# Kernel optimization log

Measured on AMD Instinct MI355X. Metric: run time of the kernel, lower is better.

## Reference

```python
import jax, jax.numpy as jnp
import numpy as np

B, NA, NMAX, NC = 32, 8400, 32, 80
TOPK, ALPHA, BETA, EPS, BG_IDX = 13, 1.0, 6.0, 1e-9, 80
IMG = 640.0


def _ciou(box1, box2, eps=1e-7):
    # box1: (b, nmax, 1, 4) xyxy, box2: (b, 1, na, 4) xyxy -> CIoU (b, nmax, na)
    b1_x1, b1_y1, b1_x2, b1_y2 = (box1[..., 0], box1[..., 1], box1[..., 2], box1[..., 3])
    b2_x1, b2_y1, b2_x2, b2_y2 = (box2[..., 0], box2[..., 1], box2[..., 2], box2[..., 3])
    inter = (jnp.minimum(b1_x2, b2_x2) - jnp.maximum(b1_x1, b2_x1)).clip(0) * \
            (jnp.minimum(b1_y2, b2_y2) - jnp.maximum(b1_y1, b2_y1)).clip(0)
    w1, h1 = b1_x2 - b1_x1, b1_y2 - b1_y1 + eps
    w2, h2 = b2_x2 - b2_x1, b2_y2 - b2_y1 + eps
    union = w1 * h1 + w2 * h2 - inter + eps
    iou = inter / union
    cw = jnp.maximum(b1_x2, b2_x2) - jnp.minimum(b1_x1, b2_x1)
    ch = jnp.maximum(b1_y2, b2_y2) - jnp.minimum(b1_y1, b2_y1)
    c2 = cw * cw + ch * ch + eps
    rho2 = ((b2_x1 + b2_x2 - b1_x1 - b1_x2) ** 2 + (b2_y1 + b2_y2 - b1_y1 - b1_y2) ** 2) / 4.0
    v = (4.0 / np.pi ** 2) * (jnp.arctan(w2 / h2) - jnp.arctan(w1 / h1)) ** 2
    alpha = jax.lax.stop_gradient(v / (v - iou + (1.0 + eps)))
    return iou - (rho2 / c2 + v * alpha)


def _rand_boxes(key, shape):
    # well-formed xyxy boxes inside a 640x640 image
    k1, k2 = jax.random.split(key)
    xy = jax.random.uniform(k1, shape[:-1] + (2,), jnp.float32) * (IMG - 64.0)
    wh = jax.random.uniform(k2, shape[:-1] + (2,), jnp.float32) * 56.0 + 8.0
    return jnp.concatenate([xy, xy + wh], axis=-1)


def setup_inputs() -> dict:
    key = jax.random.key(0)
    ks = jax.random.split(key, 6)
    pd_scores = jax.random.uniform(ks[0], (B, NA, NC), jnp.float32)
    pd_bboxes = _rand_boxes(ks[1], (B, NA, 4))
    anc_points = jax.random.uniform(ks[2], (NA, 2), jnp.float32) * IMG
    gt_labels = jax.random.randint(ks[3], (B, NMAX, 1), 0, NC, dtype=jnp.int32)
    gt_bboxes = _rand_boxes(ks[4], (B, NMAX, 4))
    mask_gt = jnp.ones((B, NMAX, 1), jnp.float32)
    return {"pd_scores": pd_scores, "pd_bboxes": pd_bboxes, "anc_points": anc_points,
            "gt_labels": gt_labels, "gt_bboxes": gt_bboxes, "mask_gt": mask_gt}


def reference(pd_scores, pd_bboxes, anc_points, gt_labels, gt_bboxes, mask_gt):
    b, na, nc = pd_scores.shape
    nmax = gt_bboxes.shape[1]
    # pairwise CIoU between every GT and every predicted box: (b, nmax, na)
    overlaps = _ciou(gt_bboxes[:, :, None, :], pd_bboxes[:, None, :, :])
    # gather predicted class score at each GT's label: (b, nmax, na)
    p = jnp.transpose(pd_scores, (0, 2, 1))                     # (b, nc, na)
    scores = jnp.take_along_axis(p, gt_labels.astype(jnp.int32), axis=1)
    align_metric = (scores ** ALPHA) * (overlaps ** BETA)
    # top-k anchors per GT along the anchor axis, scatter to a boolean mask
    _, topk_idx = jax.lax.top_k(align_metric, TOPK)             # (b, nmax, topk)
    bi = jnp.arange(b)[:, None, None]
    gi = jnp.arange(nmax)[None, :, None]
    mask_pos = jnp.zeros((b, nmax, na), bool).at[bi, gi, topk_idx].set(True)
    target_gt_idx = jnp.argmax(mask_pos, axis=1)                # (b, na)
    fg_mask = mask_pos.sum(axis=1) > 0                          # (b, na)
    # gather assigned GT label / box per anchor
    target_labels = jnp.take_along_axis(gt_labels[..., 0].astype(jnp.int32), target_gt_idx, axis=1)
    target_bboxes = jnp.take_along_axis(gt_bboxes, target_gt_idx[..., None], axis=1)  # (b, na, 4)
    target_scores = jax.nn.one_hot(target_labels, nc, dtype=jnp.float32) * fg_mask[..., None]
    target_labels = jnp.where(fg_mask, target_labels, BG_IDX)
    # normalize target scores by mean positive overlap per anchor, clamped to [0, 1]
    mpf = mask_pos.astype(overlaps.dtype)
    pos_overlaps = jnp.clip((overlaps * mpf).sum(axis=1) / (mpf.sum(axis=1) + EPS), 0.0, 1.0)
    target_scores = target_scores * pos_overlaps[..., None]
    return target_labels, target_bboxes, target_scores, fg_mask, target_gt_idx
```

## Files before the change

kernel.cpp:

```cpp
#include <hip/hip_runtime.h>
#include <math.h>

#define BATCH 32
#define NA 8400
#define NMAX 32
#define NC 80
#define TOPK 13
#define THREADS 256
#define NF4ROW (NA / 4)
#define NPT4 9
#define TILE 128
#define NTILES 66
#define SSTRIDE 81

#define OFF_BOX 268800
#define OFF_SCR 1344000
#define OFF_FG  22848000
#define OFF_TGT 23116800
#define SCR_ELEMS (OFF_FG - OFF_SCR)
#define SCR_F4    (SCR_ELEMS / 4)
#define ZPB_M     2546

typedef float f32x4 __attribute__((ext_vector_type(4)));

__device__ __forceinline__ float ciou_f(float gx1, float gy1, float gx2, float gy2,
                                        float px1, float py1, float px2, float py2) {
    const float eps = 1e-7f;
    float iw = fmaxf(fminf(gx2, px2) - fmaxf(gx1, px1), 0.0f);
    float ih = fmaxf(fminf(gy2, py2) - fmaxf(gy1, py1), 0.0f);
    float inter = iw * ih;
    float w1 = gx2 - gx1, h1 = gy2 - gy1 + eps;
    float w2 = px2 - px1, h2 = py2 - py1 + eps;
    float uni = w1 * h1 + w2 * h2 - inter + eps;
    float iou = inter / uni;
    float cw = fmaxf(gx2, px2) - fminf(gx1, px1);
    float ch = fmaxf(gy2, py2) - fminf(gy1, py1);
    float c2 = cw * cw + ch * ch + eps;
    float dx = px1 + px2 - gx1 - gx2;
    float dy = py1 + py2 - gy1 - gy2;
    float rho2 = (dx * dx + dy * dy) / 4.0f;
    float dd = atanf(w2 / h2) - atanf(w1 / h1);
    float v = (float)(4.0 / (M_PI * M_PI)) * dd * dd;
    float alpha = v / (v - iou + (1.0f + eps));
    return iou - (rho2 / c2 + v * alpha);
}

__global__ __launch_bounds__(THREADS, 3) void metric_kernel(
    const float* __restrict__ pd_scores, const float* __restrict__ pd_bboxes,
    const int* __restrict__ gt_labels, const float* __restrict__ gt_bboxes,
    float* __restrict__ met, unsigned int* __restrict__ mask,
    float* __restrict__ zbase) {
    const int b = blockIdx.y;
    const int abase = blockIdx.x * TILE;
    const int tid = threadIdx.x;
    const int na_tile = min(TILE, NA - abase);
    const float eps = 1e-7f;

    if (tid < na_tile) mask[(size_t)b * NA + abase + tid] = 0u;

    __shared__ float ssc[TILE][SSTRIDE];
    __shared__ float4 spbox[TILE];
    __shared__ float sgx1[NMAX], sgy1[NMAX], sgx2[NMAX], sgy2[NMAX];
    __shared__ float sa1[NMAX], sat1[NMAX];
    __shared__ int   slbl[NMAX];

    if (tid < NMAX) {
        float4 g = ((const float4*)gt_bboxes)[b * NMAX + tid];
        float w1 = g.z - g.x, h1 = g.w - g.y + eps;
        sgx1[tid] = g.x; sgy1[tid] = g.y; sgx2[tid] = g.z; sgy2[tid] = g.w;
        sa1[tid]  = w1 * h1;
        sat1[tid] = atanf(w1 / h1);
        slbl[tid] = gt_labels[b * NMAX + tid];
    } else if (tid >= 128) {
        int al = tid - 128;
        if (al < na_tile)
            spbox[al] = ((const float4*)pd_bboxes)[(size_t)b * NA + abase + al];
    }

    const float4* srec4 = (const float4*)(pd_scores + ((size_t)b * NA + abase) * NC);
    const int nf4 = na_tile * 20;
    float4 r[10];
#pragma unroll
    for (int i = 0; i < 10; i++) {
        int f = tid + i * THREADS;
        if (f < nf4) r[i] = srec4[f];
    }
#pragma unroll
    for (int i = 0; i < 10; i++) {
        int f = tid + i * THREADS;
        if (f < nf4) {
            int a = f / 20, c = f % 20;
            float* d = &ssc[a][c * 4];
            d[0] = r[i].x; d[1] = r[i].y; d[2] = r[i].z; d[3] = r[i].w;
        }
    }
    __syncthreads();

    if (zbase) {
        const int bid = b * NTILES + blockIdx.x;
        const size_t zoff = (size_t)bid * ZPB_M;
        f32x4* zp = (f32x4*)zbase + zoff;
        const f32x4 z = { 0.f, 0.f, 0.f, 0.f };
#pragma unroll
        for (int i = 0; i < 10; i++) {
            int j = tid + i * THREADS;
            if (j < ZPB_M && zoff + j < SCR_F4)
                __builtin_nontemporal_store(z, zp + j);
        }
    }

    const int al = tid & (TILE - 1);
    const int gbase = (tid >> 7) * 16;
    if (al >= na_tile) return;

    float4 p = spbox[al];
    float w2 = p.z - p.x, h2 = p.w - p.y + eps;
    float a2  = w2 * h2;
    float at2 = atanf(w2 / h2);
    const size_t abs_a = (size_t)abase + al;

#pragma unroll
    for (int k = 0; k < 16; k++) {
        int gi = gbase + k;
        float gx1 = sgx1[gi], gy1 = sgy1[gi], gx2 = sgx2[gi], gy2 = sgy2[gi];
        float iw = fmaxf(fminf(gx2, p.z) - fmaxf(gx1, p.x), 0.0f);
        float ih = fmaxf(fminf(gy2, p.w) - fmaxf(gy1, p.y), 0.0f);
        float inter = iw * ih;
        float uni = sa1[gi] + a2 - inter + eps;
        float iou = inter / uni;
        float cw = fmaxf(gx2, p.z) - fminf(gx1, p.x);
        float ch = fmaxf(gy2, p.w) - fminf(gy1, p.y);
        float c2 = cw * cw + ch * ch + eps;
        float dx = p.x + p.z - gx1 - gx2;
        float dy = p.y + p.w - gy1 - gy2;
        float rho2 = (dx * dx + dy * dy) / 4.0f;
        float dd = at2 - sat1[gi];
        float v = (float)(4.0 / (M_PI * M_PI)) * dd * dd;
        float alpha = v / (v - iou + (1.0f + eps));
        float ov = iou - (rho2 / c2 + v * alpha);
        float sc = ssc[al][slbl[gi]];
        float ov2 = ov * ov;
        met[((size_t)b * NMAX + gi) * NA + abs_a] = sc * (ov2 * ov2 * ov2);
    }
}

__global__ __launch_bounds__(THREADS) void topk_kernel(
    const float* __restrict__ met, unsigned int* __restrict__ mask) {
    const int tid  = threadIdx.x;
    const int lane = tid & 63;
    const int w    = tid >> 6;
    const int bid  = blockIdx.x;
    const int b  = bid >> 5;
    const int gi = bid & 31;
    const f32x4* mrow4 = (const f32x4*)(met + ((size_t)b * NMAX + gi) * NA);

    f32x4 m4[NPT4];
#pragma unroll
    for (int j = 0; j < NPT4; j++) {
        int f = j * THREADS + tid;
        if (f < NF4ROW) m4[j] = mrow4[f];
    }

    float bv0 = -INFINITY, bv1 = -INFINITY;
    int   ba0 = 0x7FFFFFFF, ba1 = 0x7FFFFFFF;
#pragma unroll
    for (int j = 0; j < NPT4; j++) {
        int f = j * THREADS + tid;
        bool vf = (f < NF4ROW);
#pragma unroll
        for (int c = 0; c < 4; c++) {
            float v = vf ? m4[j][c] : -INFINITY;
            int   a = vf ? 4 * f + c : 0x7FFFFFFF;
            bool beats0 = (v > bv0) || (v == bv0 && a < ba0);
            bool beats1 = (v > bv1) || (v == bv1 && a < ba1);
            if (beats0) { bv1 = bv0; ba1 = ba0; bv0 = v; ba0 = a; }
            else if (beats1) { bv1 = v; ba1 = a; }
        }
    }
    bool valid1 = true;

    float rv = -INFINITY; int ra = 0x7FFFFFFF;
    for (int k = 0; k < TOPK; k++) {
        float v = bv0; int a = ba0;
#pragma unroll
        for (int s = 1; s < 64; s <<= 1) {
            float ov = __shfl_xor(v, s);
            int   oa = __shfl_xor(a, s);
            if (ov > v || (ov == v && oa < a)) { v = ov; a = oa; }
        }
        if (lane == k) { rv = v; ra = a; }
        if (ba0 == a) {
            if (valid1) { bv0 = bv1; ba0 = ba1; valid1 = false; }
            else {
                float nv = -INFINITY; int na_ = 0x7FFFFFFF;
#pragma unroll
                for (int j = 0; j < NPT4; j++) {
                    int f = j * THREADS + tid;
                    bool vf = (f < NF4ROW);
#pragma unroll
                    for (int c = 0; c < 4; c++) {
                        float mv = vf ? m4[j][c] : -INFINITY;
                        int   ma = vf ? 4 * f + c : 0x7FFFFFFF;
                        bool below = (mv < v) || (mv == v && ma > a);
                        bool beats = (mv > nv) || (mv == nv && ma < na_);
                        if (below && beats && vf) { nv = mv; na_ = ma; }
                    }
                }
                bv0 = nv; ba0 = na_;
            }
        }
    }

    __shared__ float lv[4 * TOPK];
    __shared__ int   la[4 * TOPK];
    if (lane < TOPK) { lv[w * TOPK + lane] = rv; la[w * TOPK + lane] = ra; }
    __syncthreads();

    if (w == 0) {
        float v = (lane < 4 * TOPK) ? lv[lane] : -INFINITY;
        int   a = (lane < 4 * TOPK) ? la[lane] : 0x7FFFFFFF;
        for (int k = 0; k < TOPK; k++) {
            float wv = v; int wa = a;
#pragma unroll
            for (int s = 1; s < 64; s <<= 1) {
                float ov = __shfl_xor(wv, s);
                int   oa = __shfl_xor(wa, s);
                if (ov > wv || (ov == wv && oa < wa)) { wv = ov; wa = oa; }
            }
            if (lane == 0) atomicOr(&mask[(size_t)b * NA + wa], 1u << gi);
            if (a == wa) { v = -INFINITY; a = 0x7FFFFFFF; }
        }
    }
}

__global__ __launch_bounds__(THREADS) void zero_scr_kernel(float* __restrict__ out) {
    f32x4* p = (f32x4*)(out + OFF_SCR);
    const f32x4 z = { 0.f, 0.f, 0.f, 0.f };
    const int stride = gridDim.x * THREADS;
    for (int i = blockIdx.x * THREADS + threadIdx.x; i < SCR_F4; i += stride)
        __builtin_nontemporal_store(z, p + i);
}

__global__ __launch_bounds__(THREADS) void assign_kernel(
    const float* __restrict__ pd_bboxes, const int* __restrict__ gt_labels,
    const float* __restrict__ gt_bboxes, const unsigned int* __restrict__ mask,
    float* __restrict__ out) {
    const int idx = blockIdx.x * THREADS + threadIdx.x;
    const int b = idx / NA;

    unsigned msk = mask[idx];
    int tgt = msk ? (__ffs(msk) - 1) : 0;
    float4 gb = ((const float4*)gt_bboxes)[b * NMAX + tgt];
    int lbl = gt_labels[b * NMAX + tgt];
    float4 p = ((const float4*)pd_bboxes)[idx];

    float sum = 0.0f;
    int cnt = 0;
    unsigned mm = msk;
    while (mm) {
        int i = __ffs(mm) - 1;
        mm &= mm - 1;
        float4 g = ((const float4*)gt_bboxes)[b * NMAX + i];
        sum += ciou_f(g.x, g.y, g.z, g.w, p.x, p.y, p.z, p.w);
        cnt++;
    }
    float po = fminf(fmaxf(sum / ((float)cnt + 1e-9f), 0.0f), 1.0f);

    bool fg = (msk != 0);
    __builtin_nontemporal_store(fg ? (float)lbl : 80.0f, &out[idx]);
    f32x4 gbv = { gb.x, gb.y, gb.z, gb.w };
    __builtin_nontemporal_store(gbv, (f32x4*)(out + OFF_BOX) + idx);
    __builtin_nontemporal_store(fg ? 1.0f : 0.0f, &out[OFF_FG + idx]);
    __builtin_nontemporal_store((float)tgt, &out[OFF_TGT + idx]);
    if (fg) out[OFF_SCR + (size_t)idx * NC + lbl] = po;
}

extern "C" void kernel_launch(void* const* d_in, const int* in_sizes, int n_in,
                              void* d_out, int out_size, void* d_ws, size_t ws_size,
                              hipStream_t stream) {
    const float* pd_scores = (const float*)d_in[0];
    const float* pd_bboxes = (const float*)d_in[1];
    const int*   gt_labels = (const int*)d_in[3];
    const float* gt_bboxes = (const float*)d_in[4];

    float* out = (float*)d_out;
    unsigned int* mask = (unsigned int*)d_ws;

    const size_t MASK_BYTES = (size_t)BATCH * NA * 4;
    const size_t MET_BYTES  = (size_t)BATCH * NMAX * NA * 4;
    const size_t met_off = (MASK_BYTES + 255) & ~(size_t)255;
    const bool ws_met = (ws_size >= met_off + MET_BYTES);

    float* met = ws_met ? (float*)((char*)d_ws + met_off) : out + OFF_SCR;

    dim3 g1(NTILES, BATCH);
    if (ws_met) {
        metric_kernel<<<g1, THREADS, 0, stream>>>(pd_scores, pd_bboxes,
                                                  gt_labels, gt_bboxes, met, mask,
                                                  out + OFF_SCR);
        topk_kernel<<<BATCH * NMAX, THREADS, 0, stream>>>(met, mask);
    } else {
        metric_kernel<<<g1, THREADS, 0, stream>>>(pd_scores, pd_bboxes,
                                                  gt_labels, gt_bboxes, met, mask,
                                                  nullptr);
        topk_kernel<<<BATCH * NMAX, THREADS, 0, stream>>>(met, mask);
        zero_scr_kernel<<<2048, THREADS, 0, stream>>>(out);
    }
    assign_kernel<<<BATCH * NA / THREADS, THREADS, 0, stream>>>(
        pd_bboxes, gt_labels, gt_bboxes, mask, out);
}
```

Measured before the change: 80.60 us.

## Halve metric kernel score staging buffer and pipeline two 64-anchor sub-tiles

The metric kernel now stages the pd_scores rows for only 64 anchors in shared memory at a time, halving the LDS footprint and raising the launch-bounds occupancy hint from 3 to 6 blocks. The second half's scores are loaded into registers while the first half is computed, then written to LDS after a barrier. Threads are remapped so each handles one anchor against 8 GTs per sub-tile instead of 16. This aims to improve occupancy and overlap global loads with compute, at the cost of extra barriers and more live registers.

```diff
diff --git a/kernel.cpp b/kernel.cpp
--- a/kernel.cpp
+++ b/kernel.cpp
@@ -45,7 +45,7 @@
     return iou - (rho2 / c2 + v * alpha);
 }
 
-__global__ __launch_bounds__(THREADS, 3) void metric_kernel(
+__global__ __launch_bounds__(THREADS, 6) void metric_kernel(
     const float* __restrict__ pd_scores, const float* __restrict__ pd_bboxes,
     const int* __restrict__ gt_labels, const float* __restrict__ gt_bboxes,
     float* __restrict__ met, unsigned int* __restrict__ mask,
@@ -54,11 +54,13 @@
     const int abase = blockIdx.x * TILE;
     const int tid = threadIdx.x;
     const int na_tile = min(TILE, NA - abase);
+    const int n0 = min(64, na_tile);
+    const int n1 = na_tile - n0;
     const float eps = 1e-7f;
 
     if (tid < na_tile) mask[(size_t)b * NA + abase + tid] = 0u;
 
-    __shared__ float ssc[TILE][SSTRIDE];
+    __shared__ float ssc[64][SSTRIDE];
     __shared__ float4 spbox[TILE];
     __shared__ float sgx1[NMAX], sgy1[NMAX], sgx2[NMAX], sgy2[NMAX];
     __shared__ float sa1[NMAX], sat1[NMAX];
@@ -78,23 +80,32 @@
     }
 
     const float4* srec4 = (const float4*)(pd_scores + ((size_t)b * NA + abase) * NC);
-    const int nf4 = na_tile * 20;
-    float4 r[10];
-#pragma unroll
-    for (int i = 0; i < 10; i++) {
+    const int nf0 = n0 * 20;
+    float4 r[5];
+#pragma unroll
+    for (int i = 0; i < 5; i++) {
         int f = tid + i * THREADS;
-        if (f < nf4) r[i] = srec4[f];
-    }
-#pragma unroll
-    for (int i = 0; i < 10; i++) {
+        if (f < nf0) r[i] = srec4[f];
+    }
+    __syncthreads();
+#pragma unroll
+    for (int i = 0; i < 5; i++) {
         int f = tid + i * THREADS;
-        if (f < nf4) {
+        if (f < nf0) {
             int a = f / 20, c = f % 20;
             float* d = &ssc[a][c * 4];
             d[0] = r[i].x; d[1] = r[i].y; d[2] = r[i].z; d[3] = r[i].w;
         }
     }
-    __syncthreads();
+
+    const int nf1 = n1 * 20;
+    const float4* srec4b = srec4 + 64 * 20;
+    float4 r2[5];
+#pragma unroll
+    for (int i = 0; i < 5; i++) {
+        int f = tid + i * THREADS;
+        if (f < nf1) r2[i] = srec4b[f];
+    }
 
     if (zbase) {
         const int bid = b * NTILES + blockIdx.x;
@@ -108,39 +119,84 @@
                 __builtin_nontemporal_store(z, zp + j);
         }
     }
-
-    const int al = tid & (TILE - 1);
-    const int gbase = (tid >> 7) * 16;
-    if (al >= na_tile) return;
-
-    float4 p = spbox[al];
-    float w2 = p.z - p.x, h2 = p.w - p.y + eps;
-    float a2  = w2 * h2;
-    float at2 = atanf(w2 / h2);
-    const size_t abs_a = (size_t)abase + al;
-
-#pragma unroll
-    for (int k = 0; k < 16; k++) {
-        int gi = gbase + k;
-        float gx1 = sgx1[gi], gy1 = sgy1[gi], gx2 = sgx2[gi], gy2 = sgy2[gi];
-        float iw = fmaxf(fminf(gx2, p.z) - fmaxf(gx1, p.x), 0.0f);
-        float ih = fmaxf(fminf(gy2, p.w) - fmaxf(gy1, p.y), 0.0f);
-        float inter = iw * ih;
-        float uni = sa1[gi] + a2 - inter + eps;
-        float iou = inter / uni;
-        float cw = fmaxf(gx2, p.z) - fminf(gx1, p.x);
-        float ch = fmaxf(gy2, p.w) - fminf(gy1, p.y);
-        float c2 = cw * cw + ch * ch + eps;
-        float dx = p.x + p.z - gx1 - gx2;
-        float dy = p.y + p.w - gy1 - gy2;
-        float rho2 = (dx * dx + dy * dy) / 4.0f;
-        float dd = at2 - sat1[gi];
-        float v = (float)(4.0 / (M_PI * M_PI)) * dd * dd;
-        float alpha = v / (v - iou + (1.0f + eps));
-        float ov = iou - (rho2 / c2 + v * alpha);
-        float sc = ssc[al][slbl[gi]];
-        float ov2 = ov * ov;
-        met[((size_t)b * NMAX + gi) * NA + abs_a] = sc * (ov2 * ov2 * ov2);
+    __syncthreads();
+
+    const int al = tid & 63;
+    const int gbase = (tid >> 6) * 8;
+
+    if (al < n0) {
+        float4 p = spbox[al];
+        float w2 = p.z - p.x, h2 = p.w - p.y + eps;
+        float a2  = w2 * h2;
+        float at2 = atanf(w2 / h2);
+        const size_t abs_a = (size_t)abase + al;
+#pragma unroll
+        for (int k = 0; k < 8; k++) {
+            int gi = gbase + k;
+            float gx1 = sgx1[gi], gy1 = sgy1[gi], gx2 = sgx2[gi], gy2 = sgy2[gi];
+            float iw = fmaxf(fminf(gx2, p.z) - fmaxf(gx1, p.x), 0.0f);
+            float ih = fmaxf(fminf(gy2, p.w) - fmaxf(gy1, p.y), 0.0f);
+            float inter = iw * ih;
+            float uni = sa1[gi] + a2 - inter + eps;
+            float iou = inter / uni;
+            float cw = fmaxf(gx2, p.z) - fminf(gx1, p.x);
+            float ch = fmaxf(gy2, p.w) - fminf(gy1, p.y);
+            float c2 = cw * cw + ch * ch + eps;
+            float dx = p.x + p.z - gx1 - gx2;
+            float dy = p.y + p.w - gy1 - gy2;
+            float rho2 = (dx * dx + dy * dy) / 4.0f;
+            float dd = at2 - sat1[gi];
+            float v = (float)(4.0 / (M_PI * M_PI)) * dd * dd;
+            float alpha = v / (v - iou + (1.0f + eps));
+            float ov = iou - (rho2 / c2 + v * alpha);
+            float sc = ssc[al][slbl[gi]];
+            float ov2 = ov * ov;
+            met[((size_t)b * NMAX + gi) * NA + abs_a] = sc * (ov2 * ov2 * ov2);
+        }
+    }
+    if (n1 <= 0) return;
+    __syncthreads();
+
+#pragma unroll
+    for (int i = 0; i < 5; i++) {
+        int f = tid + i * THREADS;
+        if (f < nf1) {
+            int a = f / 20, c = f % 20;
+            float* d = &ssc[a][c * 4];
+            d[0] = r2[i].x; d[1] = r2[i].y; d[2] = r2[i].z; d[3] = r2[i].w;
+        }
+    }
+    __syncthreads();
+
+    if (al < n1) {
+        float4 p = spbox[64 + al];
+        float w2 = p.z - p.x, h2 = p.w - p.y + eps;
+        float a2  = w2 * h2;
+        float at2 = atanf(w2 / h2);
+        const size_t abs_a = (size_t)abase + 64 + al;
+#pragma unroll
+        for (int k = 0; k < 8; k++) {
+            int gi = gbase + k;
+            float gx1 = sgx1[gi], gy1 = sgy1[gi], gx2 = sgx2[gi], gy2 = sgy2[gi];
+            float iw = fmaxf(fminf(gx2, p.z) - fmaxf(gx1, p.x), 0.0f);
+            float ih = fmaxf(fminf(gy2, p.w) - fmaxf(gy1, p.y), 0.0f);
+            float inter = iw * ih;
+            float uni = sa1[gi] + a2 - inter + eps;
+            float iou = inter / uni;
+            float cw = fmaxf(gx2, p.z) - fminf(gx1, p.x);
+            float ch = fmaxf(gy2, p.w) - fminf(gy1, p.y);
+            float c2 = cw * cw + ch * ch + eps;
+            float dx = p.x + p.z - gx1 - gx2;
+            float dy = p.y + p.w - gy1 - gy2;
+            float rho2 = (dx * dx + dy * dy) / 4.0f;
+            float dd = at2 - sat1[gi];
+            float v = (float)(4.0 / (M_PI * M_PI)) * dd * dd;
+            float alpha = v / (v - iou + (1.0f + eps));
+            float ov = iou - (rho2 / c2 + v * alpha);
+            float sc = ssc[al][slbl[gi]];
+            float ov2 = ov * ov;
+            met[((size_t)b * NMAX + gi) * NA + abs_a] = sc * (ov2 * ov2 * ov2);
+        }
     }
 }
 
```

Result: no change. 80.66 us (+0.1%).
